# Performance work log

Hardware: AMD Instinct MI355X
Metric: run time of the kernel (lower is better)

## Reference

```python
import jax, jax.numpy as jnp
import numpy as np

NEG_INF = -9e15
ALPHA = 0.2  # LeakyReLU negative slope

N = 8192
D_IN = 512
D_OUT = 256


def setup_inputs() -> dict:
    key = jax.random.key(0)
    k1, k2, k3, k4, k5 = jax.random.split(key, 5)
    features = jax.random.normal(k1, (N, D_IN), dtype=jnp.float32)
    adjacency_matrix = jax.random.randint(k2, (N, N), 0, 2, dtype=jnp.int32)
    # learned params (torch Linear stores [out, in]; we use [in, out] layout)
    s_phi = 1.0 / np.sqrt(D_IN)
    W_phi = jax.random.uniform(k3, (D_IN, D_OUT), jnp.float32, -s_phi, s_phi)
    s_v = 1.0 / np.sqrt(D_OUT)
    w_mu = jax.random.uniform(k4, (D_OUT,), jnp.float32, -s_v, s_v)
    w_xi = jax.random.uniform(k5, (D_OUT,), jnp.float32, -s_v, s_v)
    return {"features": features, "adjacency_matrix": adjacency_matrix,
            "W_phi": W_phi, "w_mu": w_mu, "w_xi": w_xi}


def reference(features, adjacency_matrix, W_phi, w_mu, w_xi):
    h = features @ W_phi                                   # [N, d_out]
    mu = h @ w_mu                                          # [N]
    xi = h @ w_xi                                          # [N]
    e = mu[:, None] + xi[None, :]                          # [N, N] additive scores
    e = jnp.where(e >= 0, e, ALPHA * e)                    # LeakyReLU
    e = jnp.where(adjacency_matrix > 0, e, NEG_INF)        # mask non-edges
    a = jax.nn.softmax(e, axis=1)                          # row softmax (dropout p=0)
    out = a @ h                                            # weighted aggregation
    return jax.nn.elu(out)
```

## Files before the change

kernel.cpp:

```cpp
#include <hip/hip_runtime.h>
#include <cstdint>
#include <cstddef>


#define LOG2E 1.44269504f

typedef __attribute__((ext_vector_type(8))) short short8;
typedef __attribute__((ext_vector_type(4))) float floatx4;

using uint_as1 = __attribute__((address_space(1))) unsigned int;
using uint_as3 = __attribute__((address_space(3))) unsigned int;

__device__ __forceinline__ void gld_lds16(const void* g, void* l) {
  __builtin_amdgcn_global_load_lds((const uint_as1*)g, (uint_as3*)l, 16, 0, 0);
}

__device__ __forceinline__ unsigned short f2b(float f) {
  unsigned u = __float_as_uint(f);
  u += 0x7fffu + ((u >> 16) & 1u);
  return (unsigned short)(u >> 16);
}
__device__ __forceinline__ float b2f(short s) {
  return __uint_as_float(((unsigned)(unsigned short)s) << 16);
}

__global__ void k_cvt_features(const float* __restrict__ f, unsigned short* __restrict__ fb) {
  int tid = blockIdx.x * 256 + threadIdx.x;
  float4 v = ((const float4*)f)[tid];
  ushort4 o = {f2b(v.x), f2b(v.y), f2b(v.z), f2b(v.w)};
  *(ushort4*)&fb[tid * 4] = o;
}

__global__ void k_prep_wt(const float* __restrict__ w, unsigned short* __restrict__ wt) {
  int tid = blockIdx.x * 256 + threadIdx.x;
  int n = tid >> 9, k = tid & 511;
  wt[n * 512 + k] = f2b(w[k * 256 + n]);
}

__global__ void k_prep_p(const float* __restrict__ w, const float* __restrict__ wmu,
                         const float* __restrict__ wxi, float* __restrict__ pmu,
                         float* __restrict__ pxi) {
  int tid = blockIdx.x * 256 + threadIdx.x;
  int k = tid >> 2, seg = tid & 3;
  float sm = 0.f, sx = 0.f;
  int base = k * 256 + seg * 64;
#pragma unroll
  for (int c = 0; c < 64; c += 4) {
    float4 wv = *(const float4*)&w[base + c];
    float4 mv = *(const float4*)&wmu[seg * 64 + c];
    float4 xv = *(const float4*)&wxi[seg * 64 + c];
    sm += wv.x * mv.x + wv.y * mv.y + wv.z * mv.z + wv.w * mv.w;
    sx += wv.x * xv.x + wv.y * xv.y + wv.z * xv.z + wv.w * xv.w;
  }
  sm += __shfl_xor(sm, 1); sm += __shfl_xor(sm, 2);
  sx += __shfl_xor(sx, 1); sx += __shfl_xor(sx, 2);
  if (seg == 0) { pmu[k] = sm; pxi[k] = sx; }
}

__global__ void k_mu_xi(const unsigned short* __restrict__ fb, const float* __restrict__ pmu,
                        const float* __restrict__ pxi, float* __restrict__ mu,
                        float* __restrict__ xi) {
  int w = threadIdx.x >> 6, l = threadIdx.x & 63;
  int i = blockIdx.x * 4 + w;
  short8 fv = *(const short8*)&fb[i * 512 + l * 8];
  float m = 0.f, x = 0.f;
#pragma unroll
  for (int c = 0; c < 8; ++c) {
    float fvf = b2f(fv[c]);
    m = fmaf(fvf, pmu[l * 8 + c], m);
    x = fmaf(fvf, pxi[l * 8 + c], x);
  }
#pragma unroll
  for (int off = 32; off > 0; off >>= 1) {
    m += __shfl_xor(m, off);
    x += __shfl_xor(x, off);
  }
  if (l == 0) { mu[i] = m * LOG2E; xi[i] = x * LOG2E; }
}

__global__ __launch_bounds__(256, 2) void k_gemm1(const unsigned short* __restrict__ fb,
                                                  const unsigned short* __restrict__ wt,
                                                  unsigned short* __restrict__ ht) {
  __shared__ __align__(16) unsigned short As[64 * 64];
  __shared__ __align__(16) unsigned short Bs[128 * 64];
  int t = threadIdx.x, w = t >> 6, l = t & 63;
  int bm = blockIdx.x >> 1, bn = blockIdx.x & 1;
  int m0 = bm * 64, n0 = bn * 128;
  int lr = l >> 3, lg = l & 7, g = lg ^ lr;
  int kg = l >> 4, ln = l & 15;
  floatx4 zero = {0.f, 0.f, 0.f, 0.f};
  floatx4 acc[4][2];
#pragma unroll
  for (int mf = 0; mf < 4; ++mf)
#pragma unroll
    for (int nf = 0; nf < 2; ++nf) acc[mf][nf] = zero;

  for (int it = 0; it < 8; ++it) {
    int k0 = it * 64;
#pragma unroll
    for (int q = 0; q < 2; ++q) {
      int row = w * 16 + q * 8 + lr;
      const void* gp = fb + (size_t)(m0 + row) * 512 + k0 + g * 8;
      int lb = __builtin_amdgcn_readfirstlane((w * 16 + q * 8) * 64);
      gld_lds16(gp, &As[lb]);
    }
#pragma unroll
    for (int q = 0; q < 4; ++q) {
      int row = w * 32 + q * 8 + lr;
      const void* gp = wt + (size_t)(n0 + row) * 512 + k0 + g * 8;
      int lb = __builtin_amdgcn_readfirstlane((w * 32 + q * 8) * 64);
      gld_lds16(gp, &Bs[lb]);
    }
    __syncthreads();
#pragma unroll
    for (int ks = 0; ks < 2; ++ks) {
      int gg = ks * 4 + kg;
      int swz = (gg ^ (ln & 7)) * 8;
      short8 bfr[2];
#pragma unroll
      for (int nf = 0; nf < 2; ++nf)
        bfr[nf] = *(const short8*)&Bs[(w * 32 + nf * 16 + ln) * 64 + swz];
#pragma unroll
      for (int mf = 0; mf < 4; ++mf) {
        short8 afr = *(const short8*)&As[(mf * 16 + ln) * 64 + swz];
#pragma unroll
        for (int nf = 0; nf < 2; ++nf)
          acc[mf][nf] = __builtin_amdgcn_mfma_f32_16x16x32_bf16(afr, bfr[nf], acc[mf][nf], 0, 0, 0);
      }
    }
    __syncthreads();
  }
#pragma unroll
  for (int mf = 0; mf < 4; ++mf)
#pragma unroll
    for (int nf = 0; nf < 2; ++nf) {
      int ng = n0 + w * 32 + nf * 16 + ln;
      int mg = m0 + mf * 16 + kg * 4;
      ushort4 o = {f2b(acc[mf][nf][0]), f2b(acc[mf][nf][1]),
                   f2b(acc[mf][nf][2]), f2b(acc[mf][nf][3])};
      *(ushort4*)&ht[(size_t)ng * 8192 + mg] = o;
    }
}

__global__ void k_zero(float* __restrict__ num, float* __restrict__ zbuf) {
  int b = blockIdx.x, t = threadIdx.x;
  if (b < 2048) {
    float4 z4 = {0.f, 0.f, 0.f, 0.f};
    *(float4*)&num[(b * 256 + t) * 4] = z4;
  } else {
    zbuf[(b - 2048) * 256 + t] = 0.f;
  }
}

__global__ __launch_bounds__(256, 2) void k_attn4(const int* __restrict__ adj,
                                                  const unsigned short* __restrict__ ht,
                                                  const float* __restrict__ mu,
                                                  const float* __restrict__ xi,
                                                  float* __restrict__ num,
                                                  float* __restrict__ zbuf) {
  __shared__ __align__(16) unsigned short Bs[2][256 * 64];
  __shared__ __align__(16) unsigned short Ws[64 * 64];

  int t = threadIdx.x, w = t >> 6, l = t & 63;
  int ln = l & 15, kg = l >> 4;
  int lr = l >> 3, lg = l & 7, g = lg ^ lr;
  int bi = blockIdx.x & 127, bj = blockIdx.x >> 7;
  int i0 = bi * 64;
  size_t jw = (size_t)bj * 2048;

  int wi = t >> 2;
  int js = (t & 3) * 16;
  int g0 = (t & 3) * 2;
  int p0i = (g0 ^ (wi & 7)) * 8;
  int p1i = ((g0 + 1) ^ (wi & 7)) * 8;
  float mu_s = mu[i0 + wi];
  const int* arow = adj + (size_t)(i0 + wi) * 8192 + jw + js;
  const float* xrow = xi + jw + js;
  float zacc = 0.f;

  floatx4 zero = {0.f, 0.f, 0.f, 0.f};
  floatx4 acc[4][4];
#pragma unroll
  for (int mf = 0; mf < 4; ++mf)
#pragma unroll
    for (int nf = 0; nf < 4; ++nf) acc[mf][nf] = zero;

  int4 A0, A1, A2, A3;
  {
    int4 c0 = *(const int4*)(arow + 0);
    int4 c1 = *(const int4*)(arow + 4);
    int4 c2 = *(const int4*)(arow + 8);
    int4 c3 = *(const int4*)(arow + 12);
    float4 x0 = *(const float4*)(xrow + 0);
    float4 x1 = *(const float4*)(xrow + 4);
    float4 x2 = *(const float4*)(xrow + 8);
    float4 x3 = *(const float4*)(xrow + 12);
#pragma unroll
    for (int q = 0; q < 8; ++q) {
      int row = w * 64 + q * 8;
      const void* gp = ht + (size_t)(row + lr) * 8192 + jw + g * 8;
      int lb = __builtin_amdgcn_readfirstlane(row * 64);
      gld_lds16(gp, &Bs[0][lb]);
    }
    A0 = *(const int4*)(arow + 64);
    A1 = *(const int4*)(arow + 68);
    A2 = *(const int4*)(arow + 72);
    A3 = *(const int4*)(arow + 76);
    int am[16] = {c0.x, c0.y, c0.z, c0.w, c1.x, c1.y, c1.z, c1.w,
                  c2.x, c2.y, c2.z, c2.w, c3.x, c3.y, c3.z, c3.w};
    float xv[16] = {x0.x, x0.y, x0.z, x0.w, x1.x, x1.y, x1.z, x1.w,
                    x2.x, x2.y, x2.z, x2.w, x3.x, x3.y, x3.z, x3.w};
    short8 pk0, pk1;
#pragma unroll
    for (int e = 0; e < 16; ++e) {
      float s = mu_s + xv[e];
      s = fmaxf(s, 0.2f * s);
      float ev = __builtin_amdgcn_exp2f(s);
      float wv = (am[e] != 0) ? ev : 0.f;
      zacc += wv;
      if (e < 8) pk0[e] = (short)f2b(wv); else pk1[e - 8] = (short)f2b(wv);
    }
    *(short8*)&Ws[wi * 64 + p0i] = pk0;
    *(short8*)&Ws[wi * 64 + p1i] = pk1;
  }
  __syncthreads();

  for (int c = 0; c < 32; ++c) {
    int buf = c & 1, nb = buf ^ 1;
    float4 x0, x1, x2, x3;
    int4 N0, N1, N2, N3;
    if (c < 31) {
      int jo1 = (c + 1) * 64;
#pragma unroll
      for (int q = 0; q < 8; ++q) {
        int row = w * 64 + q * 8;
        const void* gp = ht + (size_t)(row + lr) * 8192 + jw + jo1 + g * 8;
        int lb = __builtin_amdgcn_readfirstlane(nb * (256 * 64) + row * 64);
        gld_lds16(gp, &Bs[0][lb]);
      }
      x0 = *(const float4*)(xrow + jo1);
      x1 = *(const float4*)(xrow + jo1 + 4);
      x2 = *(const float4*)(xrow + jo1 + 8);
      x3 = *(const float4*)(xrow + jo1 + 12);
      int jo2 = (c < 30) ? (c + 2) * 64 : 64;
      N0 = *(const int4*)(arow + jo2);
      N1 = *(const int4*)(arow + jo2 + 4);
      N2 = *(const int4*)(arow + jo2 + 8);
      N3 = *(const int4*)(arow + jo2 + 12);
    }
#pragma unroll
    for (int ks = 0; ks < 2; ++ks) {
      int swz = ((ks * 4 + kg) ^ (ln & 7)) * 8;
      short8 af[4], bf[4];
#pragma unroll
      for (int mf = 0; mf < 4; ++mf)
        af[mf] = *(const short8*)&Ws[(mf * 16 + ln) * 64 + swz];
#pragma unroll
      for (int nf = 0; nf < 4; ++nf)
        bf[nf] = *(const short8*)&Bs[buf][(w * 64 + nf * 16 + ln) * 64 + swz];
#pragma unroll
      for (int mf = 0; mf < 4; ++mf)
#pragma unroll
        for (int nf = 0; nf < 4; ++nf)
          acc[mf][nf] = __builtin_amdgcn_mfma_f32_16x16x32_bf16(af[mf], bf[nf], acc[mf][nf], 0, 0, 0);
    }
    __syncthreads();
    if (c < 31) {
      int am[16] = {A0.x, A0.y, A0.z, A0.w, A1.x, A1.y, A1.z, A1.w,
                    A2.x, A2.y, A2.z, A2.w, A3.x, A3.y, A3.z, A3.w};
      float xv[16] = {x0.x, x0.y, x0.z, x0.w, x1.x, x1.y, x1.z, x1.w,
                      x2.x, x2.y, x2.z, x2.w, x3.x, x3.y, x3.z, x3.w};
      short8 pk0, pk1;
#pragma unroll
      for (int e = 0; e < 16; ++e) {
        float s = mu_s + xv[e];
        s = fmaxf(s, 0.2f * s);
        float ev = __builtin_amdgcn_exp2f(s);
        float wv = (am[e] != 0) ? ev : 0.f;
        zacc += wv;
        if (e < 8) pk0[e] = (short)f2b(wv); else pk1[e - 8] = (short)f2b(wv);
      }
      *(short8*)&Ws[wi * 64 + p0i] = pk0;
      *(short8*)&Ws[wi * 64 + p1i] = pk1;
      A0 = N0; A1 = N1; A2 = N2; A3 = N3;
    }
    __syncthreads();
  }

  zacc += __shfl_xor(zacc, 1);
  zacc += __shfl_xor(zacc, 2);
  if ((t & 3) == 0) atomicAdd(&zbuf[i0 + wi], zacc);

#pragma unroll
  for (int mf = 0; mf < 4; ++mf)
#pragma unroll
    for (int nf = 0; nf < 4; ++nf) {
      int col = w * 64 + nf * 16 + ln;
#pragma unroll
      for (int r = 0; r < 4; ++r) {
        int row = i0 + mf * 16 + kg * 4 + r;
        atomicAdd(&num[(size_t)row * 256 + col], acc[mf][nf][r]);
      }
    }
}

__global__ void k_final(const float* __restrict__ num, const float* __restrict__ zbuf,
                        float* __restrict__ out) {
  int tid = blockIdx.x * 256 + threadIdx.x;
  int i = tid >> 6;
  float zi = 1.0f / zbuf[i];
  float4 v = *(const float4*)&num[tid * 4];
  v.x *= zi; v.y *= zi; v.z *= zi; v.w *= zi;
  v.x = (v.x > 0.f) ? v.x : (__builtin_amdgcn_exp2f(v.x * LOG2E) - 1.f);
  v.y = (v.y > 0.f) ? v.y : (__builtin_amdgcn_exp2f(v.y * LOG2E) - 1.f);
  v.z = (v.z > 0.f) ? v.z : (__builtin_amdgcn_exp2f(v.z * LOG2E) - 1.f);
  v.w = (v.w > 0.f) ? v.w : (__builtin_amdgcn_exp2f(v.w * LOG2E) - 1.f);
  *(float4*)&out[tid * 4] = v;
}

extern "C" void kernel_launch(void* const* d_in, const int* in_sizes, int n_in,
                              void* d_out, int out_size, void* d_ws, size_t ws_size,
                              hipStream_t stream) {
  const float* features = (const float*)d_in[0];
  const int* adjm = (const int*)d_in[1];
  const float* W_phi = (const float*)d_in[2];
  const float* w_mu = (const float*)d_in[3];
  const float* w_xi = (const float*)d_in[4];
  float* out = (float*)d_out;

  char* ws = (char*)d_ws;
  unsigned short* fb  = (unsigned short*)(ws + 0);
  unsigned short* ht  = (unsigned short*)(ws + 8388608);
  unsigned short* wt  = (unsigned short*)(ws + 12582912);
  float* pmu = (float*)(ws + 12845056);
  float* pxi = (float*)(ws + 12847104);
  float* muv = (float*)(ws + 12849152);
  float* xiv = (float*)(ws + 12881920);
  float* num  = (float*)(ws + 0);
  float* zbuf = (float*)(ws + 12582912);

  k_cvt_features<<<4096, 256, 0, stream>>>(features, fb);
  k_prep_wt<<<512, 256, 0, stream>>>(W_phi, wt);
  k_prep_p<<<8, 256, 0, stream>>>(W_phi, w_mu, w_xi, pmu, pxi);
  k_mu_xi<<<2048, 256, 0, stream>>>(fb, pmu, pxi, muv, xiv);
  k_gemm1<<<256, 256, 0, stream>>>(fb, wt, ht);
  k_zero<<<2080, 256, 0, stream>>>(num, zbuf);
  k_attn4<<<512, 256, 0, stream>>>(adjm, ht, muv, xiv, num, zbuf);
  k_final<<<2048, 256, 0, stream>>>(num, zbuf, out);
}
```

Before: 476.2 us.

## Pack adjacency matrix into bitmask in separate pass before attention kernel

Adds a pre-pass that uses wavefront ballots to turn the int32 adjacency matrix into a 64-bit-per-word bitmask. The attention kernel then reads one 16-bit mask word per 16 columns instead of four int4 loads, and the register prefetch of the next adjacency chunk is dropped. The 256MB adjacency matrix is still read once by the new pass, so attention-time load pressure moves into a separate streaming kernel plus an extra small write and read of the mask. The mask load inside the loop is no longer prefetched two chunks ahead and may expose some latency.

```diff
diff --git a/kernel.cpp b/kernel.cpp
--- a/kernel.cpp
+++ b/kernel.cpp
@@ -22,6 +22,26 @@
 }
 __device__ __forceinline__ float b2f(short s) {
   return __uint_as_float(((unsigned)(unsigned short)s) << 16);
+}
+
+__global__ void k_bitmask(const int* __restrict__ adj, unsigned long long* __restrict__ bm) {
+  int gw = (blockIdx.x * 256 + threadIdx.x) >> 6;
+  int lane = threadIdx.x & 63;
+  size_t w0 = (size_t)gw * 128;
+  for (int r = 0; r < 128; r += 4) {
+    size_t wd = w0 + r;
+    int v0 = adj[(wd + 0) * 64 + lane];
+    int v1 = adj[(wd + 1) * 64 + lane];
+    int v2 = adj[(wd + 2) * 64 + lane];
+    int v3 = adj[(wd + 3) * 64 + lane];
+    unsigned long long m0 = __ballot(v0 != 0);
+    unsigned long long m1 = __ballot(v1 != 0);
+    unsigned long long m2 = __ballot(v2 != 0);
+    unsigned long long m3 = __ballot(v3 != 0);
+    if (lane == 0) {
+      bm[wd] = m0; bm[wd + 1] = m1; bm[wd + 2] = m2; bm[wd + 3] = m3;
+    }
+  }
 }
 
 __global__ void k_cvt_features(const float* __restrict__ f, unsigned short* __restrict__ fb) {
@@ -84,8 +104,8 @@
   __shared__ __align__(16) unsigned short As[64 * 64];
   __shared__ __align__(16) unsigned short Bs[128 * 64];
   int t = threadIdx.x, w = t >> 6, l = t & 63;
-  int bm = blockIdx.x >> 1, bn = blockIdx.x & 1;
-  int m0 = bm * 64, n0 = bn * 128;
+  int bm_ = blockIdx.x >> 1, bn = blockIdx.x & 1;
+  int m0 = bm_ * 64, n0 = bn * 128;
   int lr = l >> 3, lg = l & 7, g = lg ^ lr;
   int kg = l >> 4, ln = l & 15;
   floatx4 zero = {0.f, 0.f, 0.f, 0.f};
@@ -152,7 +172,7 @@
   }
 }
 
-__global__ __launch_bounds__(256, 2) void k_attn4(const int* __restrict__ adj,
+__global__ __launch_bounds__(256, 2) void k_attn5(const unsigned short* __restrict__ bm16,
                                                   const unsigned short* __restrict__ ht,
                                                   const float* __restrict__ mu,
                                                   const float* __restrict__ xi,
@@ -174,7 +194,7 @@
   int p0i = (g0 ^ (wi & 7)) * 8;
   int p1i = ((g0 + 1) ^ (wi & 7)) * 8;
   float mu_s = mu[i0 + wi];
-  const int* arow = adj + (size_t)(i0 + wi) * 8192 + jw + js;
+  const unsigned short* brow = bm16 + (size_t)(i0 + wi) * 512 + (jw + js) / 16;
   const float* xrow = xi + jw + js;
   float zacc = 0.f;
 
@@ -185,12 +205,8 @@
 #pragma unroll
     for (int nf = 0; nf < 4; ++nf) acc[mf][nf] = zero;
 
-  int4 A0, A1, A2, A3;
   {
-    int4 c0 = *(const int4*)(arow + 0);
-    int4 c1 = *(const int4*)(arow + 4);
-    int4 c2 = *(const int4*)(arow + 8);
-    int4 c3 = *(const int4*)(arow + 12);
+    unsigned bits = brow[0];
     float4 x0 = *(const float4*)(xrow + 0);
     float4 x1 = *(const float4*)(xrow + 4);
     float4 x2 = *(const float4*)(xrow + 8);
@@ -202,12 +218,6 @@
       int lb = __builtin_amdgcn_readfirstlane(row * 64);
       gld_lds16(gp, &Bs[0][lb]);
     }
-    A0 = *(const int4*)(arow + 64);
-    A1 = *(const int4*)(arow + 68);
-    A2 = *(const int4*)(arow + 72);
-    A3 = *(const int4*)(arow + 76);
-    int am[16] = {c0.x, c0.y, c0.z, c0.w, c1.x, c1.y, c1.z, c1.w,
-                  c2.x, c2.y, c2.z, c2.w, c3.x, c3.y, c3.z, c3.w};
     float xv[16] = {x0.x, x0.y, x0.z, x0.w, x1.x, x1.y, x1.z, x1.w,
                     x2.x, x2.y, x2.z, x2.w, x3.x, x3.y, x3.z, x3.w};
     short8 pk0, pk1;
@@ -216,7 +226,7 @@
       float s = mu_s + xv[e];
       s = fmaxf(s, 0.2f * s);
       float ev = __builtin_amdgcn_exp2f(s);
-      float wv = (am[e] != 0) ? ev : 0.f;
+      float wv = (bits & (1u << e)) ? ev : 0.f;
       zacc += wv;
       if (e < 8) pk0[e] = (short)f2b(wv); else pk1[e - 8] = (short)f2b(wv);
     }
@@ -228,7 +238,7 @@
   for (int c = 0; c < 32; ++c) {
     int buf = c & 1, nb = buf ^ 1;
     float4 x0, x1, x2, x3;
-    int4 N0, N1, N2, N3;
+    unsigned bits = 0;
     if (c < 31) {
       int jo1 = (c + 1) * 64;
 #pragma unroll
@@ -238,15 +248,11 @@
         int lb = __builtin_amdgcn_readfirstlane(nb * (256 * 64) + row * 64);
         gld_lds16(gp, &Bs[0][lb]);
       }
+      bits = brow[(c + 1) * 4];
       x0 = *(const float4*)(xrow + jo1);
       x1 = *(const float4*)(xrow + jo1 + 4);
       x2 = *(const float4*)(xrow + jo1 + 8);
       x3 = *(const float4*)(xrow + jo1 + 12);
-      int jo2 = (c < 30) ? (c + 2) * 64 : 64;
-      N0 = *(const int4*)(arow + jo2);
-      N1 = *(const int4*)(arow + jo2 + 4);
-      N2 = *(const int4*)(arow + jo2 + 8);
-      N3 = *(const int4*)(arow + jo2 + 12);
     }
 #pragma unroll
     for (int ks = 0; ks < 2; ++ks) {
@@ -266,8 +272,6 @@
     }
     __syncthreads();
     if (c < 31) {
-      int am[16] = {A0.x, A0.y, A0.z, A0.w, A1.x, A1.y, A1.z, A1.w,
-                    A2.x, A2.y, A2.z, A2.w, A3.x, A3.y, A3.z, A3.w};
       float xv[16] = {x0.x, x0.y, x0.z, x0.w, x1.x, x1.y, x1.z, x1.w,
                       x2.x, x2.y, x2.z, x2.w, x3.x, x3.y, x3.z, x3.w};
       short8 pk0, pk1;
@@ -276,13 +280,12 @@
         float s = mu_s + xv[e];
         s = fmaxf(s, 0.2f * s);
         float ev = __builtin_amdgcn_exp2f(s);
-        float wv = (am[e] != 0) ? ev : 0.f;
+        float wv = (bits & (1u << e)) ? ev : 0.f;
         zacc += wv;
         if (e < 8) pk0[e] = (short)f2b(wv); else pk1[e - 8] = (short)f2b(wv);
       }
       *(short8*)&Ws[wi * 64 + p0i] = pk0;
       *(short8*)&Ws[wi * 64 + p1i] = pk1;
-      A0 = N0; A1 = N1; A2 = N2; A3 = N3;
     }
     __syncthreads();
   }
@@ -336,15 +339,17 @@
   float* pxi = (float*)(ws + 12847104);
   float* muv = (float*)(ws + 12849152);
   float* xiv = (float*)(ws + 12881920);
+  unsigned long long* bmask = (unsigned long long*)(ws + 13631488);
   float* num  = (float*)(ws + 0);
   float* zbuf = (float*)(ws + 12582912);
 
+  k_bitmask<<<2048, 256, 0, stream>>>(adjm, bmask);
   k_cvt_features<<<4096, 256, 0, stream>>>(features, fb);
   k_prep_wt<<<512, 256, 0, stream>>>(W_phi, wt);
   k_prep_p<<<8, 256, 0, stream>>>(W_phi, w_mu, w_xi, pmu, pxi);
   k_mu_xi<<<2048, 256, 0, stream>>>(fb, pmu, pxi, muv, xiv);
   k_gemm1<<<256, 256, 0, stream>>>(fb, wt, ht);
   k_zero<<<2080, 256, 0, stream>>>(num, zbuf);
-  k_attn4<<<512, 256, 0, stream>>>(adjm, ht, muv, xiv, num, zbuf);
+  k_attn5<<<512, 256, 0, stream>>>((const unsigned short*)bmask, ht, muv, xiv, num, zbuf);
   k_final<<<2048, 256, 0, stream>>>(num, zbuf, out);
 }
```

Result: slower. 489.2 us (+2.7%).
